# Kernel optimization log

Measured on AMD Instinct MI355X. Metric: run time of the kernel, lower is better.

The kernel has to match this reference:

```python
import jax, jax.numpy as jnp
import numpy as np

HEADS = 8
DIM_HEAD = 64
SCALE = DIM_HEAD ** -0.5

def setup_inputs() -> dict:
    key = jax.random.key(0)
    ks = jax.random.split(key, 6)
    b, n, m, qd, cd = 4, 2048, 2048, 256, 256
    inner = HEADS * DIM_HEAD
    return {
        "x": jax.random.normal(ks[0], (b, n, qd), jnp.float32),
        "context": jax.random.normal(ks[1], (b, m, cd), jnp.float32),
        "Wq": jax.random.normal(ks[2], (inner, qd), jnp.float32) * 0.02,
        "bq": jnp.zeros((inner,), jnp.float32),
        "Wkv": jax.random.normal(ks[3], (2 * inner, cd), jnp.float32) * 0.02,
        "bkv": jnp.zeros((2 * inner,), jnp.float32),
        "Wo": jax.random.normal(ks[4], (qd, inner), jnp.float32) * 0.02,
        "bo": jnp.zeros((qd,), jnp.float32),
    }

def reference(x, context, Wq, bq, Wkv, bkv, Wo, bo):
    b, n, _ = x.shape
    m = context.shape[1]
    inner = HEADS * DIM_HEAD
    # 1x1 conv projections == pointwise linear
    q = jnp.einsum('bnd,ed->bne', x, Wq) + bq            # [b, n, inner]
    kv = jnp.einsum('bmd,ed->bme', context, Wkv) + bkv    # [b, m, 2*inner]
    k, v = kv[..., :inner], kv[..., inner:]
    q = q.reshape(b, n, HEADS, DIM_HEAD).transpose(0, 2, 1, 3)  # [b,h,n,d]
    k = k.reshape(b, m, HEADS, DIM_HEAD).transpose(0, 2, 1, 3)
    v = v.reshape(b, m, HEADS, DIM_HEAD).transpose(0, 2, 1, 3)
    sim = jnp.einsum('bhid,bhjd->bhij', q, k) * SCALE     # [b,h,n,m]
    attn = jax.nn.softmax(sim, axis=-1)
    out = jnp.einsum('bhij,bhjd->bhid', attn, v)          # [b,h,n,d]
    out = out.transpose(0, 2, 1, 3).reshape(b, n, inner)  # [b,n,inner]
    return jnp.einsum('bne,oe->bno', out, Wo) + bo        # [b,n,query_dim]
```

## Files before the change

kernel.cpp:

```cpp
#include <hip/hip_runtime.h>
#include <hip/hip_bf16.h>

#define NB 4
#define SEQ 2048
#define NHEADS 8
#define ROWS (NB * SEQ)

typedef __attribute__((ext_vector_type(8))) short bf16x8;
typedef __attribute__((ext_vector_type(4))) short bf16x4;
typedef __attribute__((ext_vector_type(4))) float f32x4;
typedef __attribute__((ext_vector_type(16))) float f32x16;

__device__ inline short f2bf(float x) {
    union { float f; unsigned u; } v; v.f = x;
    unsigned r = v.u + 0x7FFF + ((v.u >> 16) & 1);
    return (short)(r >> 16);
}

__device__ inline unsigned pack2bf(float a, float b) {
    __hip_bfloat162 h = __float22bfloat162_rn(make_float2(a, b));
    unsigned u; __builtin_memcpy(&u, &h, 4);
    return u;
}

__device__ inline bf16x8 pack8(float4 a, float4 b) {
    union { unsigned u[4]; bf16x8 v; } r;
    r.u[0] = pack2bf(a.x, a.y);
    r.u[1] = pack2bf(a.z, a.w);
    r.u[2] = pack2bf(b.x, b.y);
    r.u[3] = pack2bf(b.z, b.w);
    return r.v;
}

__device__ inline unsigned comb2(unsigned w1, unsigned w2, float inv) {
    union { unsigned v; float f; } a, b, c, d;
    a.v = w1 << 16;          b.v = w2 << 16;
    c.v = w1 & 0xffff0000u;  d.v = w2 & 0xffff0000u;
    return pack2bf((a.f + b.f) * inv, (c.f + d.f) * inv);
}

__global__ __launch_bounds__(256) void proj(
    const float* __restrict__ x, const float* __restrict__ Wq,
    const float* __restrict__ bq, const float* __restrict__ ctx,
    const float* __restrict__ Wkv, const float* __restrict__ bkv,
    short* __restrict__ q2b, short* __restrict__ kv2b, float qscale)
{
    __shared__ short As[64 * 64];
    __shared__ short Ws[64 * 64];
    const int tid = threadIdx.x;
    const int bid = blockIdx.x;
    const int w = tid >> 6, lane = tid & 63, low = lane & 15, quad = lane >> 4;
    const int wm = w >> 1, wn = w & 1;
    const int K = 256;

    const float* A; const float* W; const float* bias;
    short* outp; int Ccols; float scale; int u;
    if (bid < 1024) {
        u = bid; A = x; W = Wq; bias = bq; outp = q2b;
        Ccols = 512; scale = qscale;
    } else {
        u = bid - 1024; A = ctx; W = Wkv; bias = bkv; outp = kv2b;
        Ccols = 1024; scale = 1.0f;
    }
    const int c0 = (u >> 7) * 64;
    const int r0 = (u & 127) * 64;

    const int srow = tid >> 2;
    const int sc = (tid & 3) * 2;

    f32x4 acc[2][2];
#pragma unroll
    for (int mt = 0; mt < 2; ++mt)
#pragma unroll
        for (int nt = 0; nt < 2; ++nt) acc[mt][nt] = (f32x4){0.f, 0.f, 0.f, 0.f};

    float4 paf[2][2], pwf[2][2];
    auto loadA = [&](int k0) {
        const float* p = A + (size_t)(r0 + srow) * K + k0 + sc * 8;
        paf[0][0] = ((const float4*)p)[0]; paf[0][1] = ((const float4*)p)[1];
        paf[1][0] = ((const float4*)p)[2]; paf[1][1] = ((const float4*)p)[3];
    };
    auto loadW = [&](int k0) {
        const float* p = W + (size_t)(c0 + srow) * K + k0 + sc * 8;
        pwf[0][0] = ((const float4*)p)[0]; pwf[0][1] = ((const float4*)p)[1];
        pwf[1][0] = ((const float4*)p)[2]; pwf[1][1] = ((const float4*)p)[3];
    };

    loadA(0); loadW(0);

    int k0 = 0;
    for (;;) {
        __syncthreads();
#pragma unroll
        for (int c = 0; c < 2; ++c) {
            const int pc = (sc + c) ^ (srow & 7);
            *(bf16x8*)(&As[srow * 64 + pc * 8]) = pack8(paf[c][0], paf[c][1]);
            *(bf16x8*)(&Ws[srow * 64 + pc * 8]) = pack8(pwf[c][0], pwf[c][1]);
        }
        __syncthreads();
        const int kn = k0 + 64;
        if (kn < K) { loadA(kn); loadW(kn); }
#pragma unroll
        for (int kh = 0; kh < 2; ++kh) {
            bf16x8 af[2], bfv[2];
#pragma unroll
            for (int t = 0; t < 2; ++t) {
                const int ra = wm * 32 + t * 16 + low;
                af[t] = *(const bf16x8*)(&As[ra * 64 + ((kh * 4 + quad) ^ (ra & 7)) * 8]);
                const int rb = wn * 32 + t * 16 + low;
                bfv[t] = *(const bf16x8*)(&Ws[rb * 64 + ((kh * 4 + quad) ^ (rb & 7)) * 8]);
            }
#pragma unroll
            for (int mt = 0; mt < 2; ++mt)
#pragma unroll
                for (int nt = 0; nt < 2; ++nt)
                    acc[mt][nt] = __builtin_amdgcn_mfma_f32_16x16x32_bf16(af[mt], bfv[nt], acc[mt][nt], 0, 0, 0);
        }
        k0 = kn;
        if (k0 >= K) break;
    }

#pragma unroll
    for (int nt = 0; nt < 2; ++nt) {
        const int col = c0 + wn * 32 + nt * 16 + low;
        const float bv = bias[col];
#pragma unroll
        for (int mt = 0; mt < 2; ++mt) {
            const size_t rbase = (size_t)(r0 + wm * 32 + mt * 16 + quad * 4);
#pragma unroll
            for (int r = 0; r < 4; ++r)
                outp[(rbase + r) * Ccols + col] = f2bf((acc[mt][nt][r] + bv) * scale);
        }
    }
}

__global__ __launch_bounds__(256) void gemm64_ocomb(
    const short* __restrict__ num, const float* __restrict__ lbuf,
    const float* __restrict__ W, const float* __restrict__ bias,
    float* __restrict__ out)
{
    const int K = 512, Ccols = 256;
    const size_t NHALF = (size_t)ROWS * 512;
    const int R8 = ROWS * 8;
    __shared__ short As[64 * 64];
    __shared__ short Ws[64 * 64];
    const int tid = threadIdx.x;
    const int w = tid >> 6, lane = tid & 63, low = lane & 15, quad = lane >> 4;
    const int wm = w >> 1, wn = w & 1;
    const int r0 = blockIdx.y * 64, c0 = blockIdx.x * 64;
    const int srow = tid >> 2;
    const int sc = (tid & 3) * 2;

    f32x4 acc[2][2];
#pragma unroll
    for (int mt = 0; mt < 2; ++mt)
#pragma unroll
        for (int nt = 0; nt < 2; ++nt) acc[mt][nt] = (f32x4){0.f, 0.f, 0.f, 0.f};

    uint4 pa1[2], pa2[2];
    float pinv;
    float4 pwf[2][2];

    auto loadA = [&](int k0) {
        const int hh = k0 >> 6;
        const int row = r0 + srow;
        pinv = lbuf[row * 8 + hh] + lbuf[R8 + row * 8 + hh];
        const short* p1 = num + (size_t)row * 512 + k0 + sc * 8;
        pa1[0] = ((const uint4*)p1)[0];
        pa1[1] = ((const uint4*)p1)[1];
        const short* p2 = p1 + NHALF;
        pa2[0] = ((const uint4*)p2)[0];
        pa2[1] = ((const uint4*)p2)[1];
    };
    auto loadW = [&](int k0) {
        const float* p = W + (size_t)(c0 + srow) * K + k0 + sc * 8;
        pwf[0][0] = ((const float4*)p)[0]; pwf[0][1] = ((const float4*)p)[1];
        pwf[1][0] = ((const float4*)p)[2]; pwf[1][1] = ((const float4*)p)[3];
    };

    loadA(0); loadW(0);

    int k0 = 0;
    for (;;) {
        __syncthreads();
        {
            const float inv = 1.f / pinv;
#pragma unroll
            for (int c = 0; c < 2; ++c) {
                const int pc = (sc + c) ^ (srow & 7);
                union { unsigned u[4]; bf16x8 v; } r;
                r.u[0] = comb2(pa1[c].x, pa2[c].x, inv);
                r.u[1] = comb2(pa1[c].y, pa2[c].y, inv);
                r.u[2] = comb2(pa1[c].z, pa2[c].z, inv);
                r.u[3] = comb2(pa1[c].w, pa2[c].w, inv);
                *(bf16x8*)(&As[srow * 64 + pc * 8]) = r.v;
                *(bf16x8*)(&Ws[srow * 64 + pc * 8]) = pack8(pwf[c][0], pwf[c][1]);
            }
        }
        __syncthreads();
        const int kn = k0 + 64;
        if (kn < K) { loadA(kn); loadW(kn); }
#pragma unroll
        for (int kh = 0; kh < 2; ++kh) {
            bf16x8 af[2], bfv[2];
#pragma unroll
            for (int t = 0; t < 2; ++t) {
                const int ra = wm * 32 + t * 16 + low;
                af[t] = *(const bf16x8*)(&As[ra * 64 + ((kh * 4 + quad) ^ (ra & 7)) * 8]);
                const int rb = wn * 32 + t * 16 + low;
                bfv[t] = *(const bf16x8*)(&Ws[rb * 64 + ((kh * 4 + quad) ^ (rb & 7)) * 8]);
            }
#pragma unroll
            for (int mt = 0; mt < 2; ++mt)
#pragma unroll
                for (int nt = 0; nt < 2; ++nt)
                    acc[mt][nt] = __builtin_amdgcn_mfma_f32_16x16x32_bf16(af[mt], bfv[nt], acc[mt][nt], 0, 0, 0);
        }
        k0 = kn;
        if (k0 >= K) break;
    }

#pragma unroll
    for (int nt = 0; nt < 2; ++nt) {
        const int col = c0 + wn * 32 + nt * 16 + low;
        const float bv = bias[col];
#pragma unroll
        for (int mt = 0; mt < 2; ++mt) {
            const size_t rbase = (size_t)(r0 + wm * 32 + mt * 16 + quad * 4);
#pragma unroll
            for (int r = 0; r < 4; ++r)
                out[(rbase + r) * Ccols + col] = acc[mt][nt][r] + bv;
        }
    }
}

#define KST 72
#define VST 72
#define PST 72

__global__ __launch_bounds__(256) void attn_mfma(
    const short* __restrict__ q2,
    const short* __restrict__ kv2,
    short* __restrict__ numb,
    float* __restrict__ lbuf)
{
    __shared__ short Ks[64 * KST];
    __shared__ short Vt[64 * VST];
    __shared__ short Ps[4][32 * PST];

    const int tid = threadIdx.x;
    const int w = tid >> 6;
    const int lane = tid & 63;
    const int l31 = lane & 31;
    const int h2 = lane >> 5;

    const int flat = blockIdx.x;
    const int h = flat & 7;
    const int rest = flat >> 3;
    const int half = rest & 1;
    const int rest2 = rest >> 1;
    const int qtile = rest2 & 15;
    const int b = rest2 >> 4;
    const int iq0 = qtile * 128;
    const int jt0 = half * 16;

    bf16x8 qr[4];
#pragma unroll
    for (int st = 0; st < 4; ++st)
        qr[st] = *(const bf16x8*)(q2 + (size_t)(b * SEQ + iq0 + w * 32 + l31) * 512
                                  + h * 64 + st * 16 + h2 * 8);

    const short* kbase = kv2 + (size_t)(b * SEQ) * 1024 + h * 64;
    const short* vbase = kbase + 512;
    short* pw = &Ps[w][0];

    float lsum = 0.f;
    f32x16 oacc[2];
#pragma unroll
    for (int dg = 0; dg < 2; ++dg)
#pragma unroll
        for (int r = 0; r < 16; ++r) oacc[dg][r] = 0.f;

    const int krow = tid >> 2;
    const int kc = (tid & 3) * 16;
    const int vk4 = (tid & 15) * 4;
    const int vd4 = (tid >> 4) * 4;

    bf16x8 pk0, pk1;
    bf16x4 pv0, pv1, pv2, pv3;
    {
        const short* ksrc = kbase + (size_t)(jt0 * 64 + krow) * 1024 + kc;
        pk0 = *(const bf16x8*)(ksrc);
        pk1 = *(const bf16x8*)(ksrc + 8);
        const short* vs = vbase + (size_t)(jt0 * 64 + vk4) * 1024 + vd4;
        pv0 = *(const bf16x4*)(vs);
        pv1 = *(const bf16x4*)(vs + 1024);
        pv2 = *(const bf16x4*)(vs + 2048);
        pv3 = *(const bf16x4*)(vs + 3072);
    }

    for (int jt = jt0; jt < jt0 + 16; ++jt) {
        __syncthreads();
        *(bf16x8*)(&Ks[krow * KST + kc]) = pk0;
        *(bf16x8*)(&Ks[krow * KST + kc + 8]) = pk1;
        {
            bf16x4 c0_, c1_, c2_, c3_;
            c0_[0] = pv0[0]; c0_[1] = pv1[0]; c0_[2] = pv2[0]; c0_[3] = pv3[0];
            c1_[0] = pv0[1]; c1_[1] = pv1[1]; c1_[2] = pv2[1]; c1_[3] = pv3[1];
            c2_[0] = pv0[2]; c2_[1] = pv1[2]; c2_[2] = pv2[2]; c2_[3] = pv3[2];
            c3_[0] = pv0[3]; c3_[1] = pv1[3]; c3_[2] = pv2[3]; c3_[3] = pv3[3];
            *(bf16x4*)(&Vt[(vd4 + 0) * VST + vk4]) = c0_;
            *(bf16x4*)(&Vt[(vd4 + 1) * VST + vk4]) = c1_;
            *(bf16x4*)(&Vt[(vd4 + 2) * VST + vk4]) = c2_;
            *(bf16x4*)(&Vt[(vd4 + 3) * VST + vk4]) = c3_;
        }
        __syncthreads();

        if (jt + 1 < jt0 + 16) {
            const short* ksrc = kbase + (size_t)((jt + 1) * 64 + krow) * 1024 + kc;
            pk0 = *(const bf16x8*)(ksrc);
            pk1 = *(const bf16x8*)(ksrc + 8);
            const short* vs = vbase + (size_t)((jt + 1) * 64 + vk4) * 1024 + vd4;
            pv0 = *(const bf16x4*)(vs);
            pv1 = *(const bf16x4*)(vs + 1024);
            pv2 = *(const bf16x4*)(vs + 2048);
            pv3 = *(const bf16x4*)(vs + 3072);
        }

#pragma unroll
        for (int kg = 0; kg < 2; ++kg) {
            f32x16 s;
#pragma unroll
            for (int r = 0; r < 16; ++r) s[r] = 0.f;
#pragma unroll
            for (int st = 0; st < 4; ++st) {
                const bf16x8 kf = *(const bf16x8*)(&Ks[(kg * 32 + l31) * KST + st * 16 + h2 * 8]);
                s = __builtin_amdgcn_mfma_f32_32x32x16_bf16(kf, qr[st], s, 0, 0, 0);
            }
#pragma unroll
            for (int g = 0; g < 4; ++g) {
                const float p0 = __builtin_amdgcn_exp2f(s[4 * g + 0]);
                const float p1 = __builtin_amdgcn_exp2f(s[4 * g + 1]);
                const float p2 = __builtin_amdgcn_exp2f(s[4 * g + 2]);
                const float p3 = __builtin_amdgcn_exp2f(s[4 * g + 3]);
                lsum += (p0 + p1) + (p2 + p3);
                uint2 u;
                u.x = pack2bf(p0, p1);
                u.y = pack2bf(p2, p3);
                *(uint2*)(&pw[l31 * PST + kg * 32 + 8 * g + 4 * h2]) = u;
            }
        }
        __builtin_amdgcn_wave_barrier();

#pragma unroll
        for (int st = 0; st < 4; ++st) {
            const bf16x8 pf = *(const bf16x8*)(&pw[l31 * PST + st * 16 + h2 * 8]);
#pragma unroll
            for (int dg = 0; dg < 2; ++dg) {
                const bf16x8 vf = *(const bf16x8*)(&Vt[(dg * 32 + l31) * VST + st * 16 + h2 * 8]);
                oacc[dg] = __builtin_amdgcn_mfma_f32_32x32x16_bf16(pf, vf, oacc[dg], 0, 0, 0);
            }
        }
        __builtin_amdgcn_wave_barrier();
    }

    lsum += __shfl_xor(lsum, 32);
    short* nb = numb + (size_t)half * ROWS * 512;
    float* lb = lbuf + (size_t)half * ROWS * 8;
    if (lane < 32)
        lb[(size_t)(b * SEQ + iq0 + w * 32 + l31) * 8 + h] = lsum;
#pragma unroll
    for (int dg = 0; dg < 2; ++dg)
#pragma unroll
        for (int r = 0; r < 16; ++r) {
            const int qrow = w * 32 + (r & 3) + 8 * (r >> 2) + 4 * h2;
            nb[(size_t)(b * SEQ + iq0 + qrow) * 512 + h * 64 + dg * 32 + l31] =
                f2bf(oacc[dg][r]);
        }
}

extern "C" void kernel_launch(void* const* d_in, const int* in_sizes, int n_in,
                              void* d_out, int out_size, void* d_ws, size_t ws_size,
                              hipStream_t stream) {
    const float* x   = (const float*)d_in[0];
    const float* ctx = (const float*)d_in[1];
    const float* Wq  = (const float*)d_in[2];
    const float* bq  = (const float*)d_in[3];
    const float* Wkv = (const float*)d_in[4];
    const float* bkv = (const float*)d_in[5];
    const float* Wo  = (const float*)d_in[6];
    const float* bo  = (const float*)d_in[7];
    float* out = (float*)d_out;

    short* q2b  = (short*)d_ws;
    short* kv2b = q2b + (size_t)ROWS * 512;
    short* numb = kv2b + (size_t)ROWS * 1024;
    float* lbuf = (float*)(numb + (size_t)2 * ROWS * 512);

    const float qscale = 0.125f * 1.44269504088896f;

    proj<<<3072, 256, 0, stream>>>(x, Wq, bq, ctx, Wkv, bkv, q2b, kv2b, qscale);
    attn_mfma<<<NB * NHEADS * (SEQ / 128) * 2, 256, 0, stream>>>(
        q2b, kv2b, numb, lbuf);
    gemm64_ocomb<<<dim3(256 / 64, ROWS / 64), 256, 0, stream>>>(
        numb, lbuf, Wo, bo, out);
}
```

Measured before the change: 172.2 us.

## Pre-convert inputs to bf16 and use 128x128 tiles in projection GEMM

Adds a separate conversion kernel that turns x, context and all weight matrices into bf16 once per call. The projection GEMM then reads bf16 directly and uses 128x128 output tiles with a 4x4 MFMA grid per wave, which reuses each loaded tile more and removes fp32 loads and per-tile conversion. The output GEMM also reads the pre-converted Wo. The cost is an extra kernel launch and an extra bf16 write-then-read of the inputs, plus higher register and LDS use per block.

```diff
diff --git a/kernel.cpp b/kernel.cpp
--- a/kernel.cpp
+++ b/kernel.cpp
@@ -21,15 +21,6 @@
     __hip_bfloat162 h = __float22bfloat162_rn(make_float2(a, b));
     unsigned u; __builtin_memcpy(&u, &h, 4);
     return u;
-}
-
-__device__ inline bf16x8 pack8(float4 a, float4 b) {
-    union { unsigned u[4]; bf16x8 v; } r;
-    r.u[0] = pack2bf(a.x, a.y);
-    r.u[1] = pack2bf(a.z, a.w);
-    r.u[2] = pack2bf(b.x, b.y);
-    r.u[3] = pack2bf(b.z, b.w);
-    return r.v;
 }
 
 __device__ inline unsigned comb2(unsigned w1, unsigned w2, float inv) {
@@ -39,81 +30,103 @@
     return pack2bf((a.f + b.f) * inv, (c.f + d.f) * inv);
 }
 
-__global__ __launch_bounds__(256) void proj(
-    const float* __restrict__ x, const float* __restrict__ Wq,
-    const float* __restrict__ bq, const float* __restrict__ ctx,
-    const float* __restrict__ Wkv, const float* __restrict__ bkv,
+__global__ __launch_bounds__(256) void cvt_all(
+    const float* __restrict__ x, const float* __restrict__ ctx,
+    const float* __restrict__ wq, const float* __restrict__ wkv,
+    const float* __restrict__ wo,
+    short* __restrict__ xb, short* __restrict__ cb, short* __restrict__ wqb,
+    short* __restrict__ wkvb, short* __restrict__ wob)
+{
+    const int i = blockIdx.x * 256 + threadIdx.x;
+    const float* src; short* dst; int off;
+    if (i < 524288)       { src = x;   dst = xb;   off = i; }
+    else if (i < 1048576) { src = ctx; dst = cb;   off = i - 524288; }
+    else if (i < 1081344) { src = wq;  dst = wqb;  off = i - 1048576; }
+    else if (i < 1146880) { src = wkv; dst = wkvb; off = i - 1081344; }
+    else                  { src = wo;  dst = wob;  off = i - 1146880; }
+    const float4 v = ((const float4*)src)[off];
+    uint2 o2;
+    o2.x = pack2bf(v.x, v.y);
+    o2.y = pack2bf(v.z, v.w);
+    *(uint2*)(dst + (size_t)off * 4) = o2;
+}
+
+__global__ __launch_bounds__(256, 3) void proj2(
+    const short* __restrict__ xb, const short* __restrict__ wqb,
+    const float* __restrict__ bq,
+    const short* __restrict__ cb, const short* __restrict__ wkvb,
+    const float* __restrict__ bkv,
     short* __restrict__ q2b, short* __restrict__ kv2b, float qscale)
 {
-    __shared__ short As[64 * 64];
-    __shared__ short Ws[64 * 64];
+    __shared__ short As[128 * 64];
+    __shared__ short Ws[128 * 64];
     const int tid = threadIdx.x;
     const int bid = blockIdx.x;
     const int w = tid >> 6, lane = tid & 63, low = lane & 15, quad = lane >> 4;
     const int wm = w >> 1, wn = w & 1;
     const int K = 256;
 
-    const float* A; const float* W; const float* bias;
-    short* outp; int Ccols; float scale; int u;
-    if (bid < 1024) {
-        u = bid; A = x; W = Wq; bias = bq; outp = q2b;
-        Ccols = 512; scale = qscale;
+    const short* A; const short* W; const float* bias;
+    short* outp; int Ccols; float scale; int rM0, c0;
+    if (bid < 512) {
+        A = cb; W = wkvb; bias = bkv; outp = kv2b; Ccols = 1024; scale = 1.0f;
+        c0 = (bid & 7) * 128; rM0 = (bid >> 3) * 128;
     } else {
-        u = bid - 1024; A = ctx; W = Wkv; bias = bkv; outp = kv2b;
-        Ccols = 1024; scale = 1.0f;
-    }
-    const int c0 = (u >> 7) * 64;
-    const int r0 = (u & 127) * 64;
-
-    const int srow = tid >> 2;
-    const int sc = (tid & 3) * 2;
-
-    f32x4 acc[2][2];
-#pragma unroll
-    for (int mt = 0; mt < 2; ++mt)
-#pragma unroll
-        for (int nt = 0; nt < 2; ++nt) acc[mt][nt] = (f32x4){0.f, 0.f, 0.f, 0.f};
-
-    float4 paf[2][2], pwf[2][2];
-    auto loadA = [&](int k0) {
-        const float* p = A + (size_t)(r0 + srow) * K + k0 + sc * 8;
-        paf[0][0] = ((const float4*)p)[0]; paf[0][1] = ((const float4*)p)[1];
-        paf[1][0] = ((const float4*)p)[2]; paf[1][1] = ((const float4*)p)[3];
-    };
-    auto loadW = [&](int k0) {
-        const float* p = W + (size_t)(c0 + srow) * K + k0 + sc * 8;
-        pwf[0][0] = ((const float4*)p)[0]; pwf[0][1] = ((const float4*)p)[1];
-        pwf[1][0] = ((const float4*)p)[2]; pwf[1][1] = ((const float4*)p)[3];
-    };
-
-    loadA(0); loadW(0);
+        const int u = bid - 512;
+        A = xb; W = wqb; bias = bq; outp = q2b; Ccols = 512; scale = qscale;
+        c0 = (u & 3) * 128; rM0 = (u >> 2) * 128;
+    }
+
+    const int srow = tid >> 3, sj = tid & 7;
+
+    f32x4 acc[4][4];
+#pragma unroll
+    for (int mt = 0; mt < 4; ++mt)
+#pragma unroll
+        for (int nt = 0; nt < 4; ++nt) acc[mt][nt] = (f32x4){0.f, 0.f, 0.f, 0.f};
+
+    bf16x8 pab[4], pwb[4];
+#pragma unroll
+    for (int c = 0; c < 4; ++c) {
+        const int row = c * 32 + srow;
+        pab[c] = *(const bf16x8*)(A + (size_t)(rM0 + row) * K + sj * 8);
+        pwb[c] = *(const bf16x8*)(W + (size_t)(c0 + row) * K + sj * 8);
+    }
 
     int k0 = 0;
     for (;;) {
         __syncthreads();
 #pragma unroll
-        for (int c = 0; c < 2; ++c) {
-            const int pc = (sc + c) ^ (srow & 7);
-            *(bf16x8*)(&As[srow * 64 + pc * 8]) = pack8(paf[c][0], paf[c][1]);
-            *(bf16x8*)(&Ws[srow * 64 + pc * 8]) = pack8(pwf[c][0], pwf[c][1]);
+        for (int c = 0; c < 4; ++c) {
+            const int row = c * 32 + srow;
+            const int pc = sj ^ (row & 7);
+            *(bf16x8*)(&As[row * 64 + pc * 8]) = pab[c];
+            *(bf16x8*)(&Ws[row * 64 + pc * 8]) = pwb[c];
         }
         __syncthreads();
         const int kn = k0 + 64;
-        if (kn < K) { loadA(kn); loadW(kn); }
+        if (kn < K) {
+#pragma unroll
+            for (int c = 0; c < 4; ++c) {
+                const int row = c * 32 + srow;
+                pab[c] = *(const bf16x8*)(A + (size_t)(rM0 + row) * K + kn + sj * 8);
+                pwb[c] = *(const bf16x8*)(W + (size_t)(c0 + row) * K + kn + sj * 8);
+            }
+        }
 #pragma unroll
         for (int kh = 0; kh < 2; ++kh) {
-            bf16x8 af[2], bfv[2];
-#pragma unroll
-            for (int t = 0; t < 2; ++t) {
-                const int ra = wm * 32 + t * 16 + low;
+            bf16x8 af[4], bfv[4];
+#pragma unroll
+            for (int t = 0; t < 4; ++t) {
+                const int ra = wm * 64 + t * 16 + low;
                 af[t] = *(const bf16x8*)(&As[ra * 64 + ((kh * 4 + quad) ^ (ra & 7)) * 8]);
-                const int rb = wn * 32 + t * 16 + low;
+                const int rb = wn * 64 + t * 16 + low;
                 bfv[t] = *(const bf16x8*)(&Ws[rb * 64 + ((kh * 4 + quad) ^ (rb & 7)) * 8]);
             }
 #pragma unroll
-            for (int mt = 0; mt < 2; ++mt)
-#pragma unroll
-                for (int nt = 0; nt < 2; ++nt)
+            for (int mt = 0; mt < 4; ++mt)
+#pragma unroll
+                for (int nt = 0; nt < 4; ++nt)
                     acc[mt][nt] = __builtin_amdgcn_mfma_f32_16x16x32_bf16(af[mt], bfv[nt], acc[mt][nt], 0, 0, 0);
         }
         k0 = kn;
@@ -121,12 +134,12 @@
     }
 
 #pragma unroll
-    for (int nt = 0; nt < 2; ++nt) {
-        const int col = c0 + wn * 32 + nt * 16 + low;
+    for (int nt = 0; nt < 4; ++nt) {
+        const int col = c0 + wn * 64 + nt * 16 + low;
         const float bv = bias[col];
 #pragma unroll
-        for (int mt = 0; mt < 2; ++mt) {
-            const size_t rbase = (size_t)(r0 + wm * 32 + mt * 16 + quad * 4);
+        for (int mt = 0; mt < 4; ++mt) {
+            const size_t rbase = (size_t)(rM0 + wm * 64 + mt * 16 + quad * 4);
 #pragma unroll
             for (int r = 0; r < 4; ++r)
                 outp[(rbase + r) * Ccols + col] = f2bf((acc[mt][nt][r] + bv) * scale);
@@ -136,7 +149,7 @@
 
 __global__ __launch_bounds__(256) void gemm64_ocomb(
     const short* __restrict__ num, const float* __restrict__ lbuf,
-    const float* __restrict__ W, const float* __restrict__ bias,
+    const short* __restrict__ W, const float* __restrict__ bias,
     float* __restrict__ out)
 {
     const int K = 512, Ccols = 256;
@@ -159,7 +172,7 @@
 
     uint4 pa1[2], pa2[2];
     float pinv;
-    float4 pwf[2][2];
+    bf16x8 pwb[2];
 
     auto loadA = [&](int k0) {
         const int hh = k0 >> 6;
@@ -173,9 +186,9 @@
         pa2[1] = ((const uint4*)p2)[1];
     };
     auto loadW = [&](int k0) {
-        const float* p = W + (size_t)(c0 + srow) * K + k0 + sc * 8;
-        pwf[0][0] = ((const float4*)p)[0]; pwf[0][1] = ((const float4*)p)[1];
-        pwf[1][0] = ((const float4*)p)[2]; pwf[1][1] = ((const float4*)p)[3];
+        const short* p = W + (size_t)(c0 + srow) * K + k0 + sc * 8;
+        pwb[0] = ((const bf16x8*)p)[0];
+        pwb[1] = ((const bf16x8*)p)[1];
     };
 
     loadA(0); loadW(0);
@@ -194,7 +207,7 @@
                 r.u[2] = comb2(pa1[c].z, pa2[c].z, inv);
                 r.u[3] = comb2(pa1[c].w, pa2[c].w, inv);
                 *(bf16x8*)(&As[srow * 64 + pc * 8]) = r.v;
-                *(bf16x8*)(&Ws[srow * 64 + pc * 8]) = pack8(pwf[c][0], pwf[c][1]);
+                *(bf16x8*)(&Ws[srow * 64 + pc * 8]) = pwb[c];
             }
         }
         __syncthreads();
@@ -392,16 +405,24 @@
     const float* bo  = (const float*)d_in[7];
     float* out = (float*)d_out;
 
-    short* q2b  = (short*)d_ws;
+    short* xb   = (short*)d_ws;
+    short* cb   = xb + (size_t)ROWS * 256;
+    short* wqb  = cb + (size_t)ROWS * 256;
+    short* wkvb = wqb + 131072;
+    short* wob  = wkvb + 262144;
+    short* q2b  = wob + 131072;
     short* kv2b = q2b + (size_t)ROWS * 512;
     short* numb = kv2b + (size_t)ROWS * 1024;
     float* lbuf = (float*)(numb + (size_t)2 * ROWS * 512);
 
     const float qscale = 0.125f * 1.44269504088896f;
 
-    proj<<<3072, 256, 0, stream>>>(x, Wq, bq, ctx, Wkv, bkv, q2b, kv2b, qscale);
+    cvt_all<<<4608, 256, 0, stream>>>(x, ctx, Wq, Wkv, Wo,
+                                      xb, cb, wqb, wkvb, wob);
+    proj2<<<768, 256, 0, stream>>>(xb, wqb, bq, cb, wkvb, bkv,
+                                   q2b, kv2b, qscale);
     attn_mfma<<<NB * NHEADS * (SEQ / 128) * 2, 256, 0, stream>>>(
         q2b, kv2b, numb, lbuf);
     gemm64_ocomb<<<dim3(256 / 64, ROWS / 64), 256, 0, stream>>>(
-        numb, lbuf, Wo, bo, out);
-}
+        numb, lbuf, wob, bo, out);
+}
```

Measured after the change: 162.0 us. 6.0% less time.
